# Kernel tuning notes

Hardware: AMD Instinct MI355X
Metric: run time of the kernel (lower is better)

The kernel has to match this reference:

```python
import jax, jax.numpy as jnp
import numpy as np
from jax.scipy.special import betaln

B, T = 4096, 8192

def setup_inputs() -> dict:
    key = jax.random.key(0)
    k_obs, k_a1, k_b1, k_a2, k_b2 = jax.random.split(key, 5)
    obs_seq = (jax.random.uniform(k_obs, (B, T)) < 0.5).astype(jnp.float32)
    # priors strictly positive, away from 0 to keep betaln finite
    alpha1 = jax.random.uniform(k_a1, (B,)) * 2.0 + 0.5
    beta1 = jax.random.uniform(k_b1, (B,)) * 2.0 + 0.5
    alpha2 = jax.random.uniform(k_a2, (B,)) * 2.0 + 0.5
    beta2 = jax.random.uniform(k_b2, (B,)) * 2.0 + 0.5
    mixweight = jnp.float32(0.4)
    return {"obs_seq": obs_seq, "alpha1": alpha1, "beta1": beta1,
            "alpha2": alpha2, "beta2": beta2, "mixweight": mixweight}

def reference(obs_seq, alpha1, beta1, alpha2, beta2, mixweight):
    # cumulative successes/failures, shifted right by one (posterior BEFORE obs t)
    cs = jnp.cumsum(obs_seq, axis=1)          # [B,T]
    cf = jnp.cumsum(1.0 - obs_seq, axis=1)    # [B,T]
    s_prev = jnp.pad(cs[:, :-1], ((0, 0), (1, 0)))  # cat([0, cs[:-1]])
    f_prev = jnp.pad(cf[:, :-1], ((0, 0), (1, 0)))
    a1 = alpha1[:, None] + s_prev
    b1 = beta1[:, None] + f_prev
    a2 = alpha2[:, None] + s_prev
    b2 = beta2[:, None] + f_prev
    clog1 = betaln(a1, b1) - betaln(alpha1, beta1)[:, None]
    clog2 = betaln(a2, b2) - betaln(alpha2, beta2)[:, None]
    bigconst = -clog1
    c1 = mixweight * jnp.exp(clog1 + bigconst)
    c2 = (1.0 - mixweight) * jnp.exp(clog2 + bigconst)
    post_mixweight = c1 / (c1 + c2)
    # stack the post_dict entries into one [5,B,T] array
    return jnp.stack([a1, b1, a2, b2, post_mixweight])
```

## Files before the change

kernel.cpp:

```cpp
#include <hip/hip_runtime.h>


#define BLOCK 256
#define VEC 4

typedef float v4f __attribute__((ext_vector_type(4)));

__global__ __launch_bounds__(BLOCK) void bbm_kernel(
    const float* __restrict__ obs,
    const float* __restrict__ alpha1, const float* __restrict__ beta1,
    const float* __restrict__ alpha2, const float* __restrict__ beta2,
    const float* __restrict__ mixw,
    float* __restrict__ out,
    int T, size_t bt)
{
    const int row  = blockIdx.x;
    const int tid  = threadIdx.x;
    const int lane = tid & 63;
    const int wid  = tid >> 6;

    __shared__ int   sPart[4];
    __shared__ float dPart[4];

    const float A1 = alpha1[row], B1 = beta1[row];
    const float A2 = alpha2[row], B2 = beta2[row];
    const float w  = mixw[0];
    const float AB1 = A1 + B1, AB2 = A2 + B2;
    const float w2 = 1.0f - w;

    const float* __restrict__ orow = obs + (size_t)row * T;
    float* __restrict__ obase = out + (size_t)row * T;

    const unsigned long long lt_mask = ((unsigned long long)1 << lane) - 1;

    int   carry_s = 0;
    float carry_d = 0.0f;

    const int EPB  = BLOCK * VEC;
    const int segs = T / EPB;

    v4f cur = *(const v4f*)(orow + tid * VEC);

    for (int seg = 0; seg < segs; ++seg) {
        const int t0 = seg * EPB + tid * VEC;

        v4f nxt;
        if (seg + 1 < segs) nxt = *(const v4f*)(orow + (seg + 1) * EPB + tid * VEC);

        int bit[VEC], sloc[VEC];
        int ts = 0;
        #pragma unroll
        for (int j = 0; j < VEC; ++j) { bit[j] = cur[j] > 0.5f; sloc[j] = ts; ts += bit[j]; }

        unsigned long long m0 = __ballot(bit[0]);
        unsigned long long m1 = __ballot(bit[1]);
        unsigned long long m2 = __ballot(bit[2]);
        unsigned long long m3 = __ballot(bit[3]);
        const int wave_excl = __builtin_popcountll(m0 & lt_mask)
                            + __builtin_popcountll(m1 & lt_mask)
                            + __builtin_popcountll(m2 & lt_mask)
                            + __builtin_popcountll(m3 & lt_mask);
        const int wave_tot  = __builtin_popcountll(m0) + __builtin_popcountll(m1)
                            + __builtin_popcountll(m2) + __builtin_popcountll(m3);
        if (lane == 0) sPart[wid] = wave_tot;
        __syncthreads();
        int prior = 0, total = 0;
        #pragma unroll
        for (int wI = 0; wI < 4; ++wI) {
            int p = sPart[wI];
            total += p;
            if (wI < wid) prior += p;
        }
        const int tbase_s = carry_s + prior + wave_excl;

        float dloc[VEC];
        float td = 0.0f;
        #pragma unroll
        for (int j = 0; j < VEC; ++j) {
            const float ft = (float)(t0 + j);
            const float fs = (float)(tbase_s + sloc[j]);
            const float fp = ft - fs;
            const float sel1 = bit[j] ? (A1 + fs) : (B1 + fp);
            const float sel2 = bit[j] ? (A2 + fs) : (B2 + fp);
            const float delta = __logf(sel2 * (AB1 + ft)) - __logf(sel1 * (AB2 + ft));
            dloc[j] = td;
            td += delta;
        }

        float incl_d = td;
        #pragma unroll
        for (int off = 1; off < 64; off <<= 1) {
            float n = __shfl_up(incl_d, off, 64);
            if (lane >= off) incl_d += n;
        }
        if (lane == 63) dPart[wid] = incl_d;
        __syncthreads();
        float priord = 0.0f, totald = 0.0f;
        #pragma unroll
        for (int wI = 0; wI < 4; ++wI) {
            float p = dPart[wI];
            totald += p;
            if (wI < wid) priord += p;
        }
        const float tbase_d = carry_d + priord + (incl_d - td);

        v4f va1, vb1, va2, vb2, vpm;
        #pragma unroll
        for (int j = 0; j < VEC; ++j) {
            const float ft = (float)(t0 + j);
            const float fs = (float)(tbase_s + sloc[j]);
            const float fp = ft - fs;
            const float d  = tbase_d + dloc[j];
            va1[j] = A1 + fs;
            vb1[j] = B1 + fp;
            va2[j] = A2 + fs;
            vb2[j] = B2 + fp;
            vpm[j] = w / (w + w2 * __expf(d));
        }
        float* p = obase + t0;
        __builtin_nontemporal_store(va1, (v4f*)(p));
        __builtin_nontemporal_store(vb1, (v4f*)(p + bt));
        __builtin_nontemporal_store(va2, (v4f*)(p + 2 * bt));
        __builtin_nontemporal_store(vb2, (v4f*)(p + 3 * bt));
        __builtin_nontemporal_store(vpm, (v4f*)(p + 4 * bt));

        carry_s += total;
        carry_d += totald;
        cur = nxt;
    }
}

extern "C" void kernel_launch(void* const* d_in, const int* in_sizes, int n_in,
                              void* d_out, int out_size, void* d_ws, size_t ws_size,
                              hipStream_t stream) {
    const float* obs    = (const float*)d_in[0];
    const float* alpha1 = (const float*)d_in[1];
    const float* beta1  = (const float*)d_in[2];
    const float* alpha2 = (const float*)d_in[3];
    const float* beta2  = (const float*)d_in[4];
    const float* mixw   = (const float*)d_in[5];

    const int Bn = in_sizes[1];
    const int Tn = in_sizes[0] / Bn;
    const size_t bt = (size_t)Bn * (size_t)Tn;

    bbm_kernel<<<Bn, BLOCK, 0, stream>>>(obs, alpha1, beta1, alpha2, beta2,
                                         mixw, (float*)d_out, Tn, bt);
}
```

Measured before the change: 759.2 us.

## Assign one wavefront per row to remove block-level scan synchronization

Each 64-lane wavefront now scans a whole row on its own, with four rows per 256-thread block, instead of a full block sharing one row. This removes the shared-memory partial sums and the two __syncthreads barriers per segment, and the running total comes from a lane-63 shuffle. Each wave now takes four times as many serial iterations per row, and each row's loads and stores are narrower per iteration, which may lower memory-level parallelism. The division is also swapped for the fast __fdividef.

Result: no change. 761.8 us (+0.3%).

```diff
diff --git a/kernel.cpp b/kernel.cpp
--- a/kernel.cpp
+++ b/kernel.cpp
@@ -3,6 +3,7 @@
 
 #define BLOCK 256
 #define VEC 4
+#define WPB 4
 
 typedef float v4f __attribute__((ext_vector_type(4)));
 
@@ -12,15 +13,13 @@
     const float* __restrict__ alpha2, const float* __restrict__ beta2,
     const float* __restrict__ mixw,
     float* __restrict__ out,
-    int T, size_t bt)
+    int T, size_t bt, int Bn)
 {
-    const int row  = blockIdx.x;
     const int tid  = threadIdx.x;
     const int lane = tid & 63;
     const int wid  = tid >> 6;
-
-    __shared__ int   sPart[4];
-    __shared__ float dPart[4];
+    const int row  = blockIdx.x * WPB + wid;
+    if (row >= Bn) return;
 
     const float A1 = alpha1[row], B1 = beta1[row];
     const float A2 = alpha2[row], B2 = beta2[row];
@@ -31,21 +30,21 @@
     const float* __restrict__ orow = obs + (size_t)row * T;
     float* __restrict__ obase = out + (size_t)row * T;
 
-    const unsigned long long lt_mask = ((unsigned long long)1 << lane) - 1;
+    const unsigned long long lt_mask = ((unsigned long long)1 << lane) - 1ull;
 
     int   carry_s = 0;
     float carry_d = 0.0f;
 
-    const int EPB  = BLOCK * VEC;
-    const int segs = T / EPB;
+    const int EPI   = 64 * VEC;
+    const int iters = T / EPI;
 
-    v4f cur = *(const v4f*)(orow + tid * VEC);
+    v4f cur = *(const v4f*)(orow + lane * VEC);
 
-    for (int seg = 0; seg < segs; ++seg) {
-        const int t0 = seg * EPB + tid * VEC;
+    for (int it = 0; it < iters; ++it) {
+        const int t0 = it * EPI + lane * VEC;
 
         v4f nxt;
-        if (seg + 1 < segs) nxt = *(const v4f*)(orow + (seg + 1) * EPB + tid * VEC);
+        if (it + 1 < iters) nxt = *(const v4f*)(orow + (it + 1) * EPI + lane * VEC);
 
         int bit[VEC], sloc[VEC];
         int ts = 0;
@@ -62,16 +61,7 @@
                             + __builtin_popcountll(m3 & lt_mask);
         const int wave_tot  = __builtin_popcountll(m0) + __builtin_popcountll(m1)
                             + __builtin_popcountll(m2) + __builtin_popcountll(m3);
-        if (lane == 0) sPart[wid] = wave_tot;
-        __syncthreads();
-        int prior = 0, total = 0;
-        #pragma unroll
-        for (int wI = 0; wI < 4; ++wI) {
-            int p = sPart[wI];
-            total += p;
-            if (wI < wid) prior += p;
-        }
-        const int tbase_s = carry_s + prior + wave_excl;
+        const int tbase_s = carry_s + wave_excl;
 
         float dloc[VEC];
         float td = 0.0f;
@@ -93,16 +83,8 @@
             float n = __shfl_up(incl_d, off, 64);
             if (lane >= off) incl_d += n;
         }
-        if (lane == 63) dPart[wid] = incl_d;
-        __syncthreads();
-        float priord = 0.0f, totald = 0.0f;
-        #pragma unroll
-        for (int wI = 0; wI < 4; ++wI) {
-            float p = dPart[wI];
-            totald += p;
-            if (wI < wid) priord += p;
-        }
-        const float tbase_d = carry_d + priord + (incl_d - td);
+        const float tbase_d = carry_d + (incl_d - td);
+        const float totald  = __shfl(incl_d, 63, 64);
 
         v4f va1, vb1, va2, vb2, vpm;
         #pragma unroll
@@ -115,7 +97,7 @@
             vb1[j] = B1 + fp;
             va2[j] = A2 + fs;
             vb2[j] = B2 + fp;
-            vpm[j] = w / (w + w2 * __expf(d));
+            vpm[j] = __fdividef(w, w + w2 * __expf(d));
         }
         float* p = obase + t0;
         __builtin_nontemporal_store(va1, (v4f*)(p));
@@ -124,7 +106,7 @@
         __builtin_nontemporal_store(vb2, (v4f*)(p + 3 * bt));
         __builtin_nontemporal_store(vpm, (v4f*)(p + 4 * bt));
 
-        carry_s += total;
+        carry_s += wave_tot;
         carry_d += totald;
         cur = nxt;
     }
@@ -144,6 +126,7 @@
     const int Tn = in_sizes[0] / Bn;
     const size_t bt = (size_t)Bn * (size_t)Tn;
 
-    bbm_kernel<<<Bn, BLOCK, 0, stream>>>(obs, alpha1, beta1, alpha2, beta2,
-                                         mixw, (float*)d_out, Tn, bt);
+    const int grid = (Bn + WPB - 1) / WPB;
+    bbm_kernel<<<grid, BLOCK, 0, stream>>>(obs, alpha1, beta1, alpha2, beta2,
+                                           mixw, (float*)d_out, Tn, bt, Bn);
 }
```

## Split work into one block per row and output plane

Applied to the files above, without the earlier changes.

Launches five blocks per row, each computing and writing only one of the five output planes. The four count planes only do the integer prefix scan, and only the mix-weight plane does the log/exp scan. This is meant to expose more parallelism and shorten each block's serial chain, at the cost of re-reading the observation row five times. It also double-buffers the shared partial-sum arrays, uses fast division, and replaces the nontemporal stores with plain stores.

After: 795.4 us. 4.8% more time.

```diff
diff --git a/kernel.cpp b/kernel.cpp
--- a/kernel.cpp
+++ b/kernel.cpp
@@ -3,6 +3,7 @@
 
 #define BLOCK 256
 #define VEC 4
+#define NW (BLOCK / 64)
 
 typedef float v4f __attribute__((ext_vector_type(4)));
 
@@ -14,119 +15,165 @@
     float* __restrict__ out,
     int T, size_t bt)
 {
-    const int row  = blockIdx.x;
-    const int tid  = threadIdx.x;
-    const int lane = tid & 63;
-    const int wid  = tid >> 6;
+    const int bid   = blockIdx.x;
+    const int row   = bid / 5;
+    const int plane = bid - row * 5;
+    const int tid   = threadIdx.x;
+    const int lane  = tid & 63;
+    const int wid   = tid >> 6;
 
-    __shared__ int   sPart[4];
-    __shared__ float dPart[4];
-
-    const float A1 = alpha1[row], B1 = beta1[row];
-    const float A2 = alpha2[row], B2 = beta2[row];
-    const float w  = mixw[0];
-    const float AB1 = A1 + B1, AB2 = A2 + B2;
-    const float w2 = 1.0f - w;
+    __shared__ int   sPart[2][NW];
+    __shared__ float dPart[2][NW];
 
     const float* __restrict__ orow = obs + (size_t)row * T;
-    float* __restrict__ obase = out + (size_t)row * T;
+    float* __restrict__ prow = out + (size_t)plane * bt + (size_t)row * T;
 
-    const unsigned long long lt_mask = ((unsigned long long)1 << lane) - 1;
+    const unsigned long long lt_mask = ((unsigned long long)1 << lane) - 1ull;
 
-    int   carry_s = 0;
-    float carry_d = 0.0f;
-
-    const int EPB  = BLOCK * VEC;
-    const int segs = T / EPB;
+    const int EPB   = BLOCK * VEC;
+    const int iters = T / EPB;
 
     v4f cur = *(const v4f*)(orow + tid * VEC);
 
-    for (int seg = 0; seg < segs; ++seg) {
-        const int t0 = seg * EPB + tid * VEC;
+    if (plane < 4) {
+        const float A1 = alpha1[row], B1 = beta1[row];
+        const float A2 = alpha2[row], B2 = beta2[row];
+        const float c0 = (plane == 0) ? A1 : (plane == 1) ? B1
+                       : (plane == 2) ? A2 : B2;
+        const bool use_s = (plane & 1) == 0;
 
-        v4f nxt;
-        if (seg + 1 < segs) nxt = *(const v4f*)(orow + (seg + 1) * EPB + tid * VEC);
+        int carry_s = 0;
+        for (int it = 0; it < iters; ++it) {
+            const int t0 = it * EPB + tid * VEC;
+            const int pb = it & 1;
 
-        int bit[VEC], sloc[VEC];
-        int ts = 0;
-        #pragma unroll
-        for (int j = 0; j < VEC; ++j) { bit[j] = cur[j] > 0.5f; sloc[j] = ts; ts += bit[j]; }
+            v4f nxt;
+            if (it + 1 < iters) nxt = *(const v4f*)(orow + (it + 1) * EPB + tid * VEC);
 
-        unsigned long long m0 = __ballot(bit[0]);
-        unsigned long long m1 = __ballot(bit[1]);
-        unsigned long long m2 = __ballot(bit[2]);
-        unsigned long long m3 = __ballot(bit[3]);
-        const int wave_excl = __builtin_popcountll(m0 & lt_mask)
-                            + __builtin_popcountll(m1 & lt_mask)
-                            + __builtin_popcountll(m2 & lt_mask)
-                            + __builtin_popcountll(m3 & lt_mask);
-        const int wave_tot  = __builtin_popcountll(m0) + __builtin_popcountll(m1)
-                            + __builtin_popcountll(m2) + __builtin_popcountll(m3);
-        if (lane == 0) sPart[wid] = wave_tot;
-        __syncthreads();
-        int prior = 0, total = 0;
-        #pragma unroll
-        for (int wI = 0; wI < 4; ++wI) {
-            int p = sPart[wI];
-            total += p;
-            if (wI < wid) prior += p;
+            int bit[VEC], sloc[VEC];
+            int ts = 0;
+            #pragma unroll
+            for (int j = 0; j < VEC; ++j) { bit[j] = cur[j] > 0.5f; sloc[j] = ts; ts += bit[j]; }
+
+            unsigned long long m0 = __ballot(bit[0]);
+            unsigned long long m1 = __ballot(bit[1]);
+            unsigned long long m2 = __ballot(bit[2]);
+            unsigned long long m3 = __ballot(bit[3]);
+            const int wave_excl = __builtin_popcountll(m0 & lt_mask)
+                                + __builtin_popcountll(m1 & lt_mask)
+                                + __builtin_popcountll(m2 & lt_mask)
+                                + __builtin_popcountll(m3 & lt_mask);
+            const int wave_tot  = __builtin_popcountll(m0) + __builtin_popcountll(m1)
+                                + __builtin_popcountll(m2) + __builtin_popcountll(m3);
+            if (lane == 0) sPart[pb][wid] = wave_tot;
+            __syncthreads();
+            int prior = 0, total = 0;
+            #pragma unroll
+            for (int wI = 0; wI < NW; ++wI) {
+                int p = sPart[pb][wI];
+                total += p;
+                if (wI < wid) prior += p;
+            }
+            const int tbase_s = carry_s + prior + wave_excl;
+
+            v4f o;
+            #pragma unroll
+            for (int j = 0; j < VEC; ++j) {
+                const float ft = (float)(t0 + j);
+                const float fs = (float)(tbase_s + sloc[j]);
+                o[j] = use_s ? (c0 + fs) : (c0 + (ft - fs));
+            }
+            *(v4f*)(prow + t0) = o;
+
+            carry_s += total;
+            cur = nxt;
         }
-        const int tbase_s = carry_s + prior + wave_excl;
+    } else {
+        const float A1 = alpha1[row], B1 = beta1[row];
+        const float A2 = alpha2[row], B2 = beta2[row];
+        const float w  = mixw[0];
+        const float AB1 = A1 + B1, AB2 = A2 + B2;
+        const float w2 = 1.0f - w;
 
-        float dloc[VEC];
-        float td = 0.0f;
-        #pragma unroll
-        for (int j = 0; j < VEC; ++j) {
-            const float ft = (float)(t0 + j);
-            const float fs = (float)(tbase_s + sloc[j]);
-            const float fp = ft - fs;
-            const float sel1 = bit[j] ? (A1 + fs) : (B1 + fp);
-            const float sel2 = bit[j] ? (A2 + fs) : (B2 + fp);
-            const float delta = __logf(sel2 * (AB1 + ft)) - __logf(sel1 * (AB2 + ft));
-            dloc[j] = td;
-            td += delta;
+        int   carry_s = 0;
+        float carry_d = 0.0f;
+
+        for (int it = 0; it < iters; ++it) {
+            const int t0 = it * EPB + tid * VEC;
+            const int pb = it & 1;
+
+            v4f nxt;
+            if (it + 1 < iters) nxt = *(const v4f*)(orow + (it + 1) * EPB + tid * VEC);
+
+            int bit[VEC], sloc[VEC];
+            int ts = 0;
+            #pragma unroll
+            for (int j = 0; j < VEC; ++j) { bit[j] = cur[j] > 0.5f; sloc[j] = ts; ts += bit[j]; }
+
+            unsigned long long m0 = __ballot(bit[0]);
+            unsigned long long m1 = __ballot(bit[1]);
+            unsigned long long m2 = __ballot(bit[2]);
+            unsigned long long m3 = __ballot(bit[3]);
+            const int wave_excl = __builtin_popcountll(m0 & lt_mask)
+                                + __builtin_popcountll(m1 & lt_mask)
+                                + __builtin_popcountll(m2 & lt_mask)
+                                + __builtin_popcountll(m3 & lt_mask);
+            const int wave_tot  = __builtin_popcountll(m0) + __builtin_popcountll(m1)
+                                + __builtin_popcountll(m2) + __builtin_popcountll(m3);
+            if (lane == 0) sPart[pb][wid] = wave_tot;
+            __syncthreads();
+            int prior = 0, total = 0;
+            #pragma unroll
+            for (int wI = 0; wI < NW; ++wI) {
+                int p = sPart[pb][wI];
+                total += p;
+                if (wI < wid) prior += p;
+            }
+            const int tbase_s = carry_s + prior + wave_excl;
+
+            float dloc[VEC];
+            float td = 0.0f;
+            #pragma unroll
+            for (int j = 0; j < VEC; ++j) {
+                const float ft = (float)(t0 + j);
+                const float fs = (float)(tbase_s + sloc[j]);
+                const float fp = ft - fs;
+                const float sel1 = bit[j] ? (A1 + fs) : (B1 + fp);
+                const float sel2 = bit[j] ? (A2 + fs) : (B2 + fp);
+                const float delta = __logf(sel2 * (AB1 + ft)) - __logf(sel1 * (AB2 + ft));
+                dloc[j] = td;
+                td += delta;
+            }
+
+            float incl_d = td;
+            #pragma unroll
+            for (int off = 1; off < 64; off <<= 1) {
+                float n = __shfl_up(incl_d, off, 64);
+                if (lane >= off) incl_d += n;
+            }
+            if (lane == 63) dPart[pb][wid] = incl_d;
+            __syncthreads();
+            float priord = 0.0f, totald = 0.0f;
+            #pragma unroll
+            for (int wI = 0; wI < NW; ++wI) {
+                float p = dPart[pb][wI];
+                totald += p;
+                if (wI < wid) priord += p;
+            }
+            const float tbase_d = carry_d + priord + (incl_d - td);
+
+            v4f o;
+            #pragma unroll
+            for (int j = 0; j < VEC; ++j) {
+                const float d = tbase_d + dloc[j];
+                o[j] = __fdividef(w, w + w2 * __expf(d));
+            }
+            *(v4f*)(prow + t0) = o;
+
+            carry_s += total;
+            carry_d += totald;
+            cur = nxt;
         }
-
-        float incl_d = td;
-        #pragma unroll
-        for (int off = 1; off < 64; off <<= 1) {
-            float n = __shfl_up(incl_d, off, 64);
-            if (lane >= off) incl_d += n;
-        }
-        if (lane == 63) dPart[wid] = incl_d;
-        __syncthreads();
-        float priord = 0.0f, totald = 0.0f;
-        #pragma unroll
-        for (int wI = 0; wI < 4; ++wI) {
-            float p = dPart[wI];
-            totald += p;
-            if (wI < wid) priord += p;
-        }
-        const float tbase_d = carry_d + priord + (incl_d - td);
-
-        v4f va1, vb1, va2, vb2, vpm;
-        #pragma unroll
-        for (int j = 0; j < VEC; ++j) {
-            const float ft = (float)(t0 + j);
-            const float fs = (float)(tbase_s + sloc[j]);
-            const float fp = ft - fs;
-            const float d  = tbase_d + dloc[j];
-            va1[j] = A1 + fs;
-            vb1[j] = B1 + fp;
-            va2[j] = A2 + fs;
-            vb2[j] = B2 + fp;
-            vpm[j] = w / (w + w2 * __expf(d));
-        }
-        float* p = obase + t0;
-        __builtin_nontemporal_store(va1, (v4f*)(p));
-        __builtin_nontemporal_store(vb1, (v4f*)(p + bt));
-        __builtin_nontemporal_store(va2, (v4f*)(p + 2 * bt));
-        __builtin_nontemporal_store(vb2, (v4f*)(p + 3 * bt));
-        __builtin_nontemporal_store(vpm, (v4f*)(p + 4 * bt));
-
-        carry_s += total;
-        carry_d += totald;
-        cur = nxt;
     }
 }
 
@@ -144,6 +191,6 @@
     const int Tn = in_sizes[0] / Bn;
     const size_t bt = (size_t)Bn * (size_t)Tn;
 
-    bbm_kernel<<<Bn, BLOCK, 0, stream>>>(obs, alpha1, beta1, alpha2, beta2,
-                                         mixw, (float*)d_out, Tn, bt);
+    bbm_kernel<<<Bn * 5, BLOCK, 0, stream>>>(obs, alpha1, beta1, alpha2, beta2,
+                                             mixw, (float*)d_out, Tn, bt);
 }
```
